# Kernel tuning notes

Hardware: AMD Instinct MI355X
Metric: run time of the kernel (lower is better)

Reference implementation:

```python
import jax, jax.numpy as jnp
import numpy as np

HIDDEN = 1024
HEADS = 8
HEAD_DIM = HIDDEN // HEADS  # 128
MAX_SEQ = 4096
MAX_TOKS = 2048
THETA = 10000.0
INIT_STD = 0.02


def setup_inputs() -> dict:
    key = jax.random.key(0)
    ks = jax.random.split(key, 8)
    B, L = 2, 4096
    hidden_states = jax.random.normal(ks[0], (B, L, HIDDEN), dtype=jnp.float32)
    attention_mask = jnp.ones((B, L), dtype=bool)
    segment_ids = jnp.sort(jax.random.randint(ks[1], (B, L), 0, 2), axis=-1).astype(jnp.int32)
    position_ids = jnp.sort(jax.random.randint(ks[2], (B, L), 0, MAX_SEQ), axis=-1).astype(jnp.int32)
    # nn.Linear weights stored (out_features, in_features), bias=False, normal(0, 0.02)
    wq = (jax.random.normal(ks[3], (HIDDEN, HIDDEN), dtype=jnp.float32) * INIT_STD)
    wk = (jax.random.normal(ks[4], (HIDDEN, HIDDEN), dtype=jnp.float32) * INIT_STD)
    wv = (jax.random.normal(ks[5], (HIDDEN, HIDDEN), dtype=jnp.float32) * INIT_STD)
    wo = (jax.random.normal(ks[6], (HIDDEN, HIDDEN), dtype=jnp.float32) * INIT_STD)
    return {
        "hidden_states": hidden_states,
        "wq": wq, "wk": wk, "wv": wv, "wo": wo,
        "attention_mask": attention_mask,
        "segment_ids": segment_ids,
        "position_ids": position_ids,
    }


def _freqs_cis(position_ids):
    # precompute_freqs_cis gathered at position_ids -> (B, L, HEAD_DIM//2) complex
    inv_freq = 1.0 / (THETA ** (jnp.arange(0, HEAD_DIM, 2, dtype=jnp.float32) / HEAD_DIM))
    ang = position_ids.astype(jnp.float32)[..., None] * inv_freq  # (B,L,D/2)
    return jax.lax.complex(jnp.cos(ang), jnp.sin(ang))


def _apply_rope(x, fc):
    # x: (B,L,H,D); fc: (B,L,D/2) complex; broadcast fc over heads
    xs = x.astype(jnp.float32).reshape(*x.shape[:-1], HEAD_DIM // 2, 2)
    xc = jax.lax.complex(xs[..., 0], xs[..., 1])  # (B,L,H,D/2)
    out = xc * fc[:, :, None, :]
    return jnp.stack([jnp.real(out), jnp.imag(out)], axis=-1).reshape(x.shape).astype(x.dtype)


def reference(hidden_states, wq, wk, wv, wo, attention_mask, segment_ids, position_ids):
    B, L, _ = hidden_states.shape
    q = (hidden_states @ wq.T).reshape(B, L, HEADS, HEAD_DIM)
    k = (hidden_states @ wk.T).reshape(B, L, HEADS, HEAD_DIM)
    v = (hidden_states @ wv.T).reshape(B, L, HEADS, HEAD_DIM)

    fc = _freqs_cis(position_ids)
    q = _apply_rope(q, fc)
    k = _apply_rope(k, fc)

    # block-causal mask: query block index >= key block index
    blk = jnp.arange(L) // MAX_TOKS
    causal = blk[:, None] >= blk[None, :]                                   # (L,L)
    seg = (segment_ids[:, :, None] == segment_ids[:, None, :])              # (B,L,L)
    mask = attention_mask[:, None, None, :] & seg[:, None, :, :] & causal[None, None, :, :]

    scale = 1.0 / np.float32(np.sqrt(HEAD_DIM))
    scores = jnp.einsum('bqhd,bkhd->bhqk', q, k) * scale                    # (B,H,L,L)
    scores = jnp.where(mask, scores, jnp.float32(-jnp.inf))
    probs = jax.nn.softmax(scores, axis=-1)
    attn = jnp.einsum('bhqk,bkhd->bqhd', probs, v).reshape(B, L, HIDDEN)
    return attn @ wo.T
```

## Files before the change

kernel.cpp:

```cpp
#include <hip/hip_runtime.h>
#include <hip/hip_bf16.h>
#include <cstdint>
#include <cstddef>
#include <type_traits>

#define HID 1024
#define HEADS 8
#define HDIM 128
#define SEQ 4096
#define BATCH 2

typedef float f32x4 __attribute__((ext_vector_type(4)));
typedef float f32x16 __attribute__((ext_vector_type(16)));
typedef short bf16x8 __attribute__((ext_vector_type(8)));
typedef unsigned short u16x8 __attribute__((ext_vector_type(8)));

typedef bf16x8 __attribute__((may_alias)) bf16x8_a;
typedef u16x8  __attribute__((may_alias)) u16x8_a;
typedef float4 __attribute__((may_alias)) float4_a;
typedef unsigned int __attribute__((may_alias)) u32_a;

__device__ __forceinline__ unsigned short f2bf(float f) {
    union { float f; unsigned int u; } v; v.f = f;
    unsigned int u = v.u;
    unsigned int r = (u + 0x7FFFu + ((u >> 16) & 1u)) >> 16;
    return (unsigned short)r;
}
__device__ __forceinline__ float bf2f(unsigned short h) {
    union { unsigned int u; float f; } v; v.u = ((unsigned int)h) << 16;
    return v.f;
}

__device__ __forceinline__ void plane_swap(unsigned int& x, unsigned int& y) {
    asm("v_permlane32_swap_b32 %0, %1" : "+v"(x), "+v"(y));
}
__device__ __forceinline__ unsigned int cvt_pk(float lo, float hi) {
    unsigned int r;
    asm("v_cvt_pk_bf16_f32 %0, %1, %2" : "=v"(r) : "v"(lo), "v"(hi));
    return r;
}
__device__ __forceinline__ bf16x8 pack4(unsigned int a, unsigned int b,
                                        unsigned int c, unsigned int d) {
    union { unsigned int u[4]; bf16x8 v; } t;
    t.u[0] = a; t.u[1] = b; t.u[2] = c; t.u[3] = d;
    return t.v;
}
__device__ __forceinline__ void g2lds16(const unsigned short* g, unsigned short* l) {
    __builtin_amdgcn_global_load_lds(
        (const __attribute__((address_space(1))) void*)g,
        (__attribute__((address_space(3))) void*)l, 16, 0, 0);
}

__global__ __launch_bounds__(256)
void cvt_kernel(const float* __restrict__ X, unsigned short* __restrict__ Y)
{
    int i = (blockIdx.x * 256 + threadIdx.x) * 8;
    float4 d0 = *(const float4_a*)&X[i];
    float4 d1 = *(const float4_a*)&X[i + 4];
    u16x8 t;
    t[0] = f2bf(d0.x); t[1] = f2bf(d0.y); t[2] = f2bf(d0.z); t[3] = f2bf(d0.w);
    t[4] = f2bf(d1.x); t[5] = f2bf(d1.y); t[6] = f2bf(d1.z); t[7] = f2bf(d1.w);
    *(u16x8_a*)&Y[i] = t;
}

__global__ __launch_bounds__(256)
void cvtw_kernel(const float* __restrict__ w0, const float* __restrict__ w1,
                 const float* __restrict__ w2, const float* __restrict__ w3,
                 unsigned short* __restrict__ Y)
{
    const int WSZ8 = (HID * HID) / 8;
    int c = blockIdx.x * 256 + threadIdx.x;
    int quarter = c >> 17;
    int idx = (c & (WSZ8 - 1)) * 8;
    const float* w = quarter == 0 ? w0 : quarter == 1 ? w1 : quarter == 2 ? w2 : w3;
    float4 d0 = *(const float4_a*)&w[idx];
    float4 d1 = *(const float4_a*)&w[idx + 4];
    u16x8 t;
    t[0] = f2bf(d0.x); t[1] = f2bf(d0.y); t[2] = f2bf(d0.z); t[3] = f2bf(d0.w);
    t[4] = f2bf(d1.x); t[5] = f2bf(d1.y); t[6] = f2bf(d1.z); t[7] = f2bf(d1.w);
    *(u16x8_a*)&Y[(size_t)quarter * HID * HID + idx] = t;
}

template<typename OutT>
__global__ __launch_bounds__(256)
void gemm_swz(const unsigned short* __restrict__ A, const unsigned short* __restrict__ B,
              OutT* __restrict__ C, int M, int N, int K, int lda)
{
    __shared__ __align__(16) unsigned short Al[128][64];
    __shared__ __align__(16) unsigned short Bl[128][64];
    const int tid  = threadIdx.x;
    const int lane = tid & 63;
    const int w    = tid >> 6;
    const int wr   = w >> 1, wc = w & 1;
    const int l16  = lane & 15, l4 = lane >> 4;
    const int nwg  = gridDim.x * gridDim.y;
    const int id   = blockIdx.y * gridDim.x + blockIdx.x;
    const int swz  = (id & 7) * (nwg >> 3) + (id >> 3);
    const int bx   = swz % gridDim.x, by = swz / gridDim.x;
    const int tm   = by * 128, tn = bx * 128;
    const int srow  = lane >> 3;
    const int sslot = (lane & 7) ^ srow;

    f32x4 acc[4][4] = {};

    for (int ko = 0; ko < K; ko += 64) {
        __syncthreads();
#pragma unroll
        for (int it = 0; it < 4; ++it) {
            int ca = w * 4 + it;
            int row = ca * 8 + srow;
            g2lds16(&A[(size_t)(tm + row) * lda + ko + sslot * 8], &Al[ca * 8][0]);
            g2lds16(&B[(size_t)(tn + row) * K   + ko + sslot * 8], &Bl[ca * 8][0]);
        }
        __syncthreads();
#pragma unroll
        for (int kk = 0; kk < 2; ++kk) {
            const int rslot = (kk * 4 + l4) ^ (l16 & 7);
            bf16x8 af[4], bfr[4];
#pragma unroll
            for (int i = 0; i < 4; ++i)
                af[i] = *(const bf16x8_a*)&Al[wr*64 + i*16 + l16][rslot * 8];
#pragma unroll
            for (int j = 0; j < 4; ++j)
                bfr[j] = *(const bf16x8_a*)&Bl[wc*64 + j*16 + l16][rslot * 8];
#pragma unroll
            for (int i = 0; i < 4; ++i)
#pragma unroll
                for (int j = 0; j < 4; ++j)
                    acc[i][j] = __builtin_amdgcn_mfma_f32_16x16x32_bf16(af[i], bfr[j], acc[i][j], 0, 0, 0);
        }
    }
#pragma unroll
    for (int i = 0; i < 4; ++i)
#pragma unroll
        for (int j = 0; j < 4; ++j)
#pragma unroll
            for (int r = 0; r < 4; ++r) {
                int row = tm + wr*64 + i*16 + l4*4 + r;
                int col = tn + wc*64 + j*16 + l16;
                if constexpr (std::is_same<OutT, float>::value)
                    C[(size_t)row * N + col] = acc[i][j][r];
                else
                    C[(size_t)row * N + col] = f2bf(acc[i][j][r]);
            }
}

template<bool A_BF16, bool B_BF16, typename OutT>
__global__ __launch_bounds__(256)
void gemm_bt(const void* __restrict__ Av, const void* __restrict__ Bv,
             OutT* __restrict__ C, int M, int N, int K, int lda)
{
    __shared__ __align__(16) unsigned short Al[128][72];
    __shared__ __align__(16) unsigned short Bl[128][72];
    const int tid  = threadIdx.x;
    const int lane = tid & 63;
    const int w    = tid >> 6;
    const int wr   = w >> 1, wc = w & 1;
    const int l16  = lane & 15, l4 = lane >> 4;
    const int tm   = blockIdx.y * 128, tn = blockIdx.x * 128;

    f32x4 acc[4][4] = {};

    for (int ko = 0; ko < K; ko += 64) {
        __syncthreads();
#pragma unroll
        for (int it = 0; it < 4; ++it) {
            int c = tid + 256 * it;
            int row = c >> 3, col0 = (c & 7) * 8;
            if constexpr (A_BF16) {
                const unsigned short* A = (const unsigned short*)Av;
                *(u16x8_a*)&Al[row][col0] =
                    *(const u16x8_a*)&A[(size_t)(tm + row) * lda + ko + col0];
            } else {
                const float* A = (const float*)Av;
                const float* p = &A[(size_t)(tm + row) * lda + ko + col0];
                float4 d0 = *(const float4_a*)p;
                float4 d1 = *(const float4_a*)(p + 4);
                u16x8 t;
                t[0] = f2bf(d0.x); t[1] = f2bf(d0.y); t[2] = f2bf(d0.z); t[3] = f2bf(d0.w);
                t[4] = f2bf(d1.x); t[5] = f2bf(d1.y); t[6] = f2bf(d1.z); t[7] = f2bf(d1.w);
                *(u16x8_a*)&Al[row][col0] = t;
            }
            if constexpr (B_BF16) {
                const unsigned short* B = (const unsigned short*)Bv;
                *(u16x8_a*)&Bl[row][col0] =
                    *(const u16x8_a*)&B[(size_t)(tn + row) * K + ko + col0];
            } else {
                const float* B = (const float*)Bv;
                const float* p = &B[(size_t)(tn + row) * K + ko + col0];
                float4 d0 = *(const float4_a*)p;
                float4 d1 = *(const float4_a*)(p + 4);
                u16x8 t;
                t[0] = f2bf(d0.x); t[1] = f2bf(d0.y); t[2] = f2bf(d0.z); t[3] = f2bf(d0.w);
                t[4] = f2bf(d1.x); t[5] = f2bf(d1.y); t[6] = f2bf(d1.z); t[7] = f2bf(d1.w);
                *(u16x8_a*)&Bl[row][col0] = t;
            }
        }
        __syncthreads();
#pragma unroll
        for (int kk = 0; kk < 2; ++kk) {
            bf16x8 af[4], bfr[4];
#pragma unroll
            for (int i = 0; i < 4; ++i)
                af[i] = *(const bf16x8_a*)&Al[wr*64 + i*16 + l16][kk*32 + l4*8];
#pragma unroll
            for (int j = 0; j < 4; ++j)
                bfr[j] = *(const bf16x8_a*)&Bl[wc*64 + j*16 + l16][kk*32 + l4*8];
#pragma unroll
            for (int i = 0; i < 4; ++i)
#pragma unroll
                for (int j = 0; j < 4; ++j)
                    acc[i][j] = __builtin_amdgcn_mfma_f32_16x16x32_bf16(af[i], bfr[j], acc[i][j], 0, 0, 0);
        }
    }
#pragma unroll
    for (int i = 0; i < 4; ++i)
#pragma unroll
        for (int j = 0; j < 4; ++j)
#pragma unroll
            for (int r = 0; r < 4; ++r) {
                int row = tm + wr*64 + i*16 + l4*4 + r;
                int col = tn + wc*64 + j*16 + l16;
                if constexpr (std::is_same<OutT, float>::value)
                    C[(size_t)row * N + col] = acc[i][j][r];
                else
                    C[(size_t)row * N + col] = f2bf(acc[i][j][r]);
            }
}

template<int NH>
__global__ __launch_bounds__(256)
void rope_kernel(unsigned short* __restrict__ X, const int* __restrict__ pos_ids, int RS)
{
    int c = blockIdx.x * 256 + threadIdx.x;
    int d0 = (c & 15) * 8;
    int l  = (c >> 4) & 4095;
    int b  = c >> 16;
    int pos = pos_ids[b * SEQ + l];
    float sth[4], cth[4];
#pragma unroll
    for (int j = 0; j < 4; ++j) {
        int i = (d0 >> 1) + j;
        float invf = powf(10000.0f, -(float)i * (1.0f / 64.0f));
        float ang = (float)pos * invf;
        sincosf(ang, &sth[j], &cth[j]);
    }
    size_t base = (size_t)(b * SEQ + l) * RS + d0;
#pragma unroll
    for (int h = 0; h < NH; ++h) {
        u16x8 d = *(const u16x8_a*)&X[base + h * HDIM];
#pragma unroll
        for (int j = 0; j < 4; ++j) {
            float x0 = bf2f(d[2*j]), x1 = bf2f(d[2*j+1]);
            d[2*j]   = f2bf(x0 * cth[j] - x1 * sth[j]);
            d[2*j+1] = f2bf(x0 * sth[j] + x1 * cth[j]);
        }
        *(u16x8_a*)&X[base + h * HDIM] = d;
    }
}

__global__ __launch_bounds__(256, 2)
void attn_kernel(const unsigned short* Q,
                 const unsigned short* K,
                 const unsigned short* V,
                 const int* __restrict__ seg,
                 unsigned short* O, int RS)
{
    __shared__ __align__(16) unsigned short Kl[2][64][136];
    __shared__ __align__(16) unsigned short Vt[2][128][72];

    const int tid  = threadIdx.x;
    const int lane = tid & 63;
    const int l32  = lane & 31, hi = lane >> 5;
    const int w    = tid >> 6;
    const int qt = (SEQ / 128 - 1) - blockIdx.x;
    const int h  = blockIdx.y;
    const int b  = blockIdx.z;
    const int qg0 = qt * 128 + w * 32;
    const int hoff = h * HDIM;

    bf16x8 qf[8];
    {
        size_t base = (size_t)(b * SEQ + qg0 + l32) * RS + hoff;
#pragma unroll
        for (int kk = 0; kk < 8; ++kk)
            qf[kk] = *(const bf16x8_a*)&Q[base + kk*16 + hi*8];
    }

    f32x16 acco0 = {}, acco1 = {}, acco2 = {}, acco3 = {};
    float lsum = 0.f;

    const int nkt = ((qt >> 4) + 1) * 32;

    int lo = 0, hb = SEQ;
    while (lo < hb) { int mid = (lo + hb) >> 1; if (seg[b * SEQ + mid] == 0) lo = mid + 1; else hb = mid; }
    const int boundary = lo;
    const bool blk_seg1 = (seg[b * SEQ + qt * 128] == 1);
    const bool blk_seg0 = (seg[b * SEQ + qt * 128 + 127] == 0);
    const bool mixed = !blk_seg0 && !blk_seg1;
    int kstart = 0, kend = nkt;
    if (blk_seg1) kstart = boundary >> 6;
    if (blk_seg0) {
        int ke = (boundary + 63) >> 6;
        kend = ke < nkt ? ke : nkt;
    }
    const bool qlt = (qg0 + l32) < boundary;

    const int kp = tid & 31, db = tid >> 5;
    const float sc = 0.08838834764831845f;

    u16x8 kreg[4], v0a, v0b, v1a, v1b;
    {
        const int kb = kstart * 64;
#pragma unroll
        for (int it = 0; it < 4; ++it) {
            int c = tid + 256 * it;
            kreg[it] = *(const u16x8_a*)&K[(size_t)(b * SEQ + kb + (c >> 4)) * RS + hoff + (c & 15) * 8];
        }
        size_t vb0 = (size_t)(b * SEQ + kb + 2 * kp) * RS + hoff + db * 16;
        size_t vb1 = (size_t)(b * SEQ + kb + 2 * kp + 1) * RS + hoff + db * 16;
        v0a = *(const u16x8_a*)&V[vb0];     v0b = *(const u16x8_a*)&V[vb0 + 8];
        v1a = *(const u16x8_a*)&V[vb1];     v1b = *(const u16x8_a*)&V[vb1 + 8];
    }
#pragma unroll
    for (int it = 0; it < 4; ++it) {
        int c = tid + 256 * it;
        *(u16x8_a*)&Kl[0][c >> 4][(c & 15) * 8] = kreg[it];
    }
#pragma unroll
    for (int j = 0; j < 8; ++j) {
        *(u32_a*)&Vt[0][db * 16 + j][2 * kp] =
            (unsigned int)(unsigned short)v0a[j] | ((unsigned int)(unsigned short)v1a[j] << 16);
        *(u32_a*)&Vt[0][db * 16 + 8 + j][2 * kp] =
            (unsigned int)(unsigned short)v0b[j] | ((unsigned int)(unsigned short)v1b[j] << 16);
    }
    if (kstart + 1 < kend) {
        const int kb2 = (kstart + 1) * 64;
#pragma unroll
        for (int it = 0; it < 4; ++it) {
            int c = tid + 256 * it;
            kreg[it] = *(const u16x8_a*)&K[(size_t)(b * SEQ + kb2 + (c >> 4)) * RS + hoff + (c & 15) * 8];
        }
        size_t vb0 = (size_t)(b * SEQ + kb2 + 2 * kp) * RS + hoff + db * 16;
        size_t vb1 = (size_t)(b * SEQ + kb2 + 2 * kp + 1) * RS + hoff + db * 16;
        v0a = *(const u16x8_a*)&V[vb0];     v0b = *(const u16x8_a*)&V[vb0 + 8];
        v1a = *(const u16x8_a*)&V[vb1];     v1b = *(const u16x8_a*)&V[vb1 + 8];
    }
    __syncthreads();

    int buf = 0;
    for (int kt = kstart; kt < kend; ++kt) {
        const int kb = kt * 64;

        f32x16 a0 = {}, a1 = {};
#pragma unroll
        for (int kk = 0; kk < 8; ++kk) {
            bf16x8 k0 = *(const bf16x8_a*)&Kl[buf][     l32][kk*16 + hi*8];
            bf16x8 k1 = *(const bf16x8_a*)&Kl[buf][32 + l32][kk*16 + hi*8];
            a0 = __builtin_amdgcn_mfma_f32_32x32x16_bf16(k0, qf[kk], a0, 0, 0, 0);
            a1 = __builtin_amdgcn_mfma_f32_32x32x16_bf16(k1, qf[kk], a1, 0, 0, 0);
        }

        unsigned int pk0[8], pk1[8];
        const bool need_mask = mixed || (kb < boundary && kb + 64 > boundary);
        if (need_mask) {
            const int kb0 = kb + 4 * hi, kb1 = kb + 32 + 4 * hi;
#pragma unroll
            for (int i = 0; i < 8; ++i) {
                int r0 = 2 * i;
                int off = (r0 & 3) + 8 * (r0 >> 2);
                float p0 = ((kb0 + off     < boundary) == qlt) ? __expf(a0[r0]     * sc) : 0.0f;
                float p1 = ((kb0 + off + 1 < boundary) == qlt) ? __expf(a0[r0 + 1] * sc) : 0.0f;
                float q0 = ((kb1 + off     < boundary) == qlt) ? __expf(a1[r0]     * sc) : 0.0f;
                float q1 = ((kb1 + off + 1 < boundary) == qlt) ? __expf(a1[r0 + 1] * sc) : 0.0f;
                lsum += (p0 + p1) + (q0 + q1);
                pk0[i] = cvt_pk(p0, p1);
                pk1[i] = cvt_pk(q0, q1);
            }
        } else {
#pragma unroll
            for (int i = 0; i < 8; ++i) {
                int r0 = 2 * i;
                float p0 = __expf(a0[r0]     * sc);
                float p1 = __expf(a0[r0 + 1] * sc);
                float q0 = __expf(a1[r0]     * sc);
                float q1 = __expf(a1[r0 + 1] * sc);
                lsum += (p0 + p1) + (q0 + q1);
                pk0[i] = cvt_pk(p0, p1);
                pk1[i] = cvt_pk(q0, q1);
            }
        }
        plane_swap(pk0[0], pk0[2]); plane_swap(pk0[1], pk0[3]);
        plane_swap(pk0[4], pk0[6]); plane_swap(pk0[5], pk0[7]);
        plane_swap(pk1[0], pk1[2]); plane_swap(pk1[1], pk1[3]);
        plane_swap(pk1[4], pk1[6]); plane_swap(pk1[5], pk1[7]);
        bf16x8 pf[4];
        pf[0] = pack4(pk0[0], pk0[1], pk0[2], pk0[3]);
        pf[1] = pack4(pk0[4], pk0[5], pk0[6], pk0[7]);
        pf[2] = pack4(pk1[0], pk1[1], pk1[2], pk1[3]);
        pf[3] = pack4(pk1[4], pk1[5], pk1[6], pk1[7]);

#pragma unroll
        for (int ks = 0; ks < 4; ++ks) {
            bf16x8 vf0 = *(const bf16x8_a*)&Vt[buf][      l32][ks*16 + hi*8];
            bf16x8 vf1 = *(const bf16x8_a*)&Vt[buf][32  + l32][ks*16 + hi*8];
            bf16x8 vf2 = *(const bf16x8_a*)&Vt[buf][64  + l32][ks*16 + hi*8];
            bf16x8 vf3 = *(const bf16x8_a*)&Vt[buf][96  + l32][ks*16 + hi*8];
            acco0 = __builtin_amdgcn_mfma_f32_32x32x16_bf16(pf[ks], vf0, acco0, 0, 0, 0);
            acco1 = __builtin_amdgcn_mfma_f32_32x32x16_bf16(pf[ks], vf1, acco1, 0, 0, 0);
            acco2 = __builtin_amdgcn_mfma_f32_32x32x16_bf16(pf[ks], vf2, acco2, 0, 0, 0);
            acco3 = __builtin_amdgcn_mfma_f32_32x32x16_bf16(pf[ks], vf3, acco3, 0, 0, 0);
        }

        if (kt + 1 < kend) {
            const int nb = buf ^ 1;
#pragma unroll
            for (int it = 0; it < 4; ++it) {
                int c = tid + 256 * it;
                *(u16x8_a*)&Kl[nb][c >> 4][(c & 15) * 8] = kreg[it];
            }
#pragma unroll
            for (int j = 0; j < 8; ++j) {
                *(u32_a*)&Vt[nb][db * 16 + j][2 * kp] =
                    (unsigned int)(unsigned short)v0a[j] | ((unsigned int)(unsigned short)v1a[j] << 16);
                *(u32_a*)&Vt[nb][db * 16 + 8 + j][2 * kp] =
                    (unsigned int)(unsigned short)v0b[j] | ((unsigned int)(unsigned short)v1b[j] << 16);
            }
            if (kt + 2 < kend) {
                const int kb2 = (kt + 2) * 64;
#pragma unroll
                for (int it = 0; it < 4; ++it) {
                    int c = tid + 256 * it;
                    kreg[it] = *(const u16x8_a*)&K[(size_t)(b * SEQ + kb2 + (c >> 4)) * RS + hoff + (c & 15) * 8];
                }
                size_t vb0 = (size_t)(b * SEQ + kb2 + 2 * kp) * RS + hoff + db * 16;
                size_t vb1 = (size_t)(b * SEQ + kb2 + 2 * kp + 1) * RS + hoff + db * 16;
                v0a = *(const u16x8_a*)&V[vb0];     v0b = *(const u16x8_a*)&V[vb0 + 8];
                v1a = *(const u16x8_a*)&V[vb1];     v1b = *(const u16x8_a*)&V[vb1 + 8];
            }
            __syncthreads();
        }
        buf ^= 1;
    }

    float tot = lsum + __shfl_xor(lsum, 32, 64);
#pragma unroll
    for (int r = 0; r < 16; ++r) {
        int qrow = (r & 3) + 8 * (r >> 2) + 4 * hi;
        float inv = 1.0f / __shfl(tot, qrow, 64);
        size_t base = (size_t)(b * SEQ + qg0 + qrow) * RS + hoff;
        O[base +       l32] = f2bf(acco0[r] * inv);
        O[base +  32 + l32] = f2bf(acco1[r] * inv);
        O[base +  64 + l32] = f2bf(acco2[r] * inv);
        O[base +  96 + l32] = f2bf(acco3[r] * inv);
    }
}

extern "C" void kernel_launch(void* const* d_in, const int* in_sizes, int n_in,
                              void* d_out, int out_size, void* d_ws, size_t ws_size,
                              hipStream_t stream)
{
    const float* X  = (const float*)d_in[0];
    const float* wq = (const float*)d_in[1];
    const float* wk = (const float*)d_in[2];
    const float* wv = (const float*)d_in[3];
    const float* wo = (const float*)d_in[4];
    const int* seg = (const int*)d_in[n_in - 2];
    const int* pos = (const int*)d_in[n_in - 1];
    float* out = (float*)d_out;

    const size_t NTOK = (size_t)BATCH * SEQ;
    const size_t MAT  = NTOK * HID;
    const size_t WSZ  = (size_t)HID * HID;

    if (ws_size >= (4 * MAT + 4 * WSZ) * sizeof(unsigned short)) {
        unsigned short* QKVb = (unsigned short*)d_ws;
        unsigned short* Xb   = QKVb + 3 * MAT;
        unsigned short* Wb   = Xb + MAT;
        unsigned short* Wob  = Wb + 3 * WSZ;

        cvt_kernel<<<(int)(MAT / (256 * 8)), 256, 0, stream>>>(X, Xb);
        cvtw_kernel<<<(int)(4 * WSZ / (256 * 8)), 256, 0, stream>>>(wq, wk, wv, wo, Wb);

        dim3 gq(3 * HID / 128, (int)(NTOK / 128));
        gemm_swz<unsigned short><<<gq, 256, 0, stream>>>(
            Xb, Wb, QKVb, (int)NTOK, 3 * HID, HID, HID);

        rope_kernel<16><<<(BATCH * SEQ * 16) / 256, 256, 0, stream>>>(QKVb, pos, 3 * HID);

        dim3 ga(SEQ / 128, HEADS, BATCH);
        attn_kernel<<<ga, 256, 0, stream>>>(QKVb, QKVb + HID, QKVb + 2 * HID, seg,
                                            QKVb , 3 * HID);

        dim3 go(HID / 128, (int)(NTOK / 128));
        gemm_swz<float><<<go, 256, 0, stream>>>(
            QKVb, Wob, out, (int)NTOK, HID, HID, 3 * HID);
    } else {
        unsigned short* Qb = (unsigned short*)d_ws;
        unsigned short* Kb = Qb + MAT;
        unsigned short* Vb = Kb + MAT;

        dim3 gg(HID / 128, (int)(NTOK / 128));
        gemm_bt<false, false, unsigned short><<<gg, 256, 0, stream>>>(
            (const void*)X, (const void*)wq, Qb, (int)NTOK, HID, HID, HID);
        gemm_bt<false, false, unsigned short><<<gg, 256, 0, stream>>>(
            (const void*)X, (const void*)wk, Kb, (int)NTOK, HID, HID, HID);
        gemm_bt<false, false, unsigned short><<<gg, 256, 0, stream>>>(
            (const void*)X, (const void*)wv, Vb, (int)NTOK, HID, HID, HID);

        rope_kernel<8><<<(BATCH * SEQ * 16) / 256, 256, 0, stream>>>(Qb, pos, HID);
        rope_kernel<8><<<(BATCH * SEQ * 16) / 256, 256, 0, stream>>>(Kb, pos, HID);

        dim3 ga(SEQ / 128, HEADS, BATCH);
        attn_kernel<<<ga, 256, 0, stream>>>(Qb, Kb, Vb, seg, Qb, HID);

        gemm_bt<true, false, float><<<gg, 256, 0, stream>>>(
            (const void*)Qb, (const void*)wo, out, (int)NTOK, HID, HID, HID);
    }
}
```

Baseline: 203.3 us.

## Split attention KV range across two blocks and merge partial outputs

Adds a split-K attention kernel where each query tile's key range is divided between two blocks, writing unnormalized bf16 partial outputs and row sums. A merge kernel then sums the halves and normalizes into the QKV buffer. This doubles grid parallelism and cuts the imbalance from long causal tiles. It also drops LDS double buffering to allow higher occupancy. The cost is extra workspace traffic, a second kernel launch, and bf16 rounding of unnormalized partials. It only runs if the workspace is large enough, otherwise the old path is kept.

```diff
diff --git a/kernel.cpp b/kernel.cpp
--- a/kernel.cpp
+++ b/kernel.cpp
@@ -259,15 +259,17 @@
     }
 }
 
-__global__ __launch_bounds__(256, 2)
-void attn_kernel(const unsigned short* Q,
-                 const unsigned short* K,
-                 const unsigned short* V,
-                 const int* __restrict__ seg,
-                 unsigned short* O, int RS)
-{
-    __shared__ __align__(16) unsigned short Kl[2][64][136];
-    __shared__ __align__(16) unsigned short Vt[2][128][72];
+__global__ __launch_bounds__(256, 4)
+void attn_split(const unsigned short* Q,
+                const unsigned short* K,
+                const unsigned short* V,
+                const int* __restrict__ seg,
+                unsigned short* __restrict__ Op,
+                float* __restrict__ Lp,
+                int RS)
+{
+    __shared__ __align__(16) unsigned short Kl[64][136];
+    __shared__ __align__(16) unsigned short Vt[128][72];
 
     const int tid  = threadIdx.x;
     const int lane = tid & 63;
@@ -275,7 +277,8 @@
     const int w    = tid >> 6;
     const int qt = (SEQ / 128 - 1) - blockIdx.x;
     const int h  = blockIdx.y;
-    const int b  = blockIdx.z;
+    const int zz = blockIdx.z;
+    const int b  = zz >> 1, half = zz & 1;
     const int qg0 = qt * 128 + w * 32;
     const int hoff = h * HDIM;
 
@@ -304,14 +307,18 @@
         int ke = (boundary + 63) >> 6;
         kend = ke < nkt ? ke : nkt;
     }
+    const int T = kend - kstart;
+    const int mid = kstart + ((T + 1) >> 1);
+    const int ks2 = half ? mid : kstart;
+    const int ke2 = half ? kend : mid;
+
     const bool qlt = (qg0 + l32) < boundary;
-
     const int kp = tid & 31, db = tid >> 5;
     const float sc = 0.08838834764831845f;
 
     u16x8 kreg[4], v0a, v0b, v1a, v1b;
-    {
-        const int kb = kstart * 64;
+    if (ks2 < ke2) {
+        const int kb = ks2 * 64;
 #pragma unroll
         for (int it = 0; it < 4; ++it) {
             int c = tid + 256 * it;
@@ -322,41 +329,42 @@
         v0a = *(const u16x8_a*)&V[vb0];     v0b = *(const u16x8_a*)&V[vb0 + 8];
         v1a = *(const u16x8_a*)&V[vb1];     v1b = *(const u16x8_a*)&V[vb1 + 8];
     }
-#pragma unroll
-    for (int it = 0; it < 4; ++it) {
-        int c = tid + 256 * it;
-        *(u16x8_a*)&Kl[0][c >> 4][(c & 15) * 8] = kreg[it];
-    }
-#pragma unroll
-    for (int j = 0; j < 8; ++j) {
-        *(u32_a*)&Vt[0][db * 16 + j][2 * kp] =
-            (unsigned int)(unsigned short)v0a[j] | ((unsigned int)(unsigned short)v1a[j] << 16);
-        *(u32_a*)&Vt[0][db * 16 + 8 + j][2 * kp] =
-            (unsigned int)(unsigned short)v0b[j] | ((unsigned int)(unsigned short)v1b[j] << 16);
-    }
-    if (kstart + 1 < kend) {
-        const int kb2 = (kstart + 1) * 64;
+
+    for (int kt = ks2; kt < ke2; ++kt) {
+        const int kb = kt * 64;
+        __syncthreads();
 #pragma unroll
         for (int it = 0; it < 4; ++it) {
             int c = tid + 256 * it;
-            kreg[it] = *(const u16x8_a*)&K[(size_t)(b * SEQ + kb2 + (c >> 4)) * RS + hoff + (c & 15) * 8];
-        }
-        size_t vb0 = (size_t)(b * SEQ + kb2 + 2 * kp) * RS + hoff + db * 16;
-        size_t vb1 = (size_t)(b * SEQ + kb2 + 2 * kp + 1) * RS + hoff + db * 16;
-        v0a = *(const u16x8_a*)&V[vb0];     v0b = *(const u16x8_a*)&V[vb0 + 8];
-        v1a = *(const u16x8_a*)&V[vb1];     v1b = *(const u16x8_a*)&V[vb1 + 8];
-    }
-    __syncthreads();
-
-    int buf = 0;
-    for (int kt = kstart; kt < kend; ++kt) {
-        const int kb = kt * 64;
+            *(u16x8_a*)&Kl[c >> 4][(c & 15) * 8] = kreg[it];
+        }
+#pragma unroll
+        for (int j = 0; j < 8; ++j) {
+            *(u32_a*)&Vt[db * 16 + j][2 * kp] =
+                (unsigned int)(unsigned short)v0a[j] | ((unsigned int)(unsigned short)v1a[j] << 16);
+            *(u32_a*)&Vt[db * 16 + 8 + j][2 * kp] =
+                (unsigned int)(unsigned short)v0b[j] | ((unsigned int)(unsigned short)v1b[j] << 16);
+        }
+        __syncthreads();
+
+        if (kt + 1 < ke2) {
+            const int kb2 = (kt + 1) * 64;
+#pragma unroll
+            for (int it = 0; it < 4; ++it) {
+                int c = tid + 256 * it;
+                kreg[it] = *(const u16x8_a*)&K[(size_t)(b * SEQ + kb2 + (c >> 4)) * RS + hoff + (c & 15) * 8];
+            }
+            size_t vb0 = (size_t)(b * SEQ + kb2 + 2 * kp) * RS + hoff + db * 16;
+            size_t vb1 = (size_t)(b * SEQ + kb2 + 2 * kp + 1) * RS + hoff + db * 16;
+            v0a = *(const u16x8_a*)&V[vb0];     v0b = *(const u16x8_a*)&V[vb0 + 8];
+            v1a = *(const u16x8_a*)&V[vb1];     v1b = *(const u16x8_a*)&V[vb1 + 8];
+        }
 
         f32x16 a0 = {}, a1 = {};
 #pragma unroll
         for (int kk = 0; kk < 8; ++kk) {
-            bf16x8 k0 = *(const bf16x8_a*)&Kl[buf][     l32][kk*16 + hi*8];
-            bf16x8 k1 = *(const bf16x8_a*)&Kl[buf][32 + l32][kk*16 + hi*8];
+            bf16x8 k0 = *(const bf16x8_a*)&Kl[     l32][kk*16 + hi*8];
+            bf16x8 k1 = *(const bf16x8_a*)&Kl[32 + l32][kk*16 + hi*8];
             a0 = __builtin_amdgcn_mfma_f32_32x32x16_bf16(k0, qf[kk], a0, 0, 0, 0);
             a1 = __builtin_amdgcn_mfma_f32_32x32x16_bf16(k1, qf[kk], a1, 0, 0, 0);
         }
@@ -402,6 +410,195 @@
 
 #pragma unroll
         for (int ks = 0; ks < 4; ++ks) {
+            bf16x8 vf0 = *(const bf16x8_a*)&Vt[      l32][ks*16 + hi*8];
+            bf16x8 vf1 = *(const bf16x8_a*)&Vt[32  + l32][ks*16 + hi*8];
+            bf16x8 vf2 = *(const bf16x8_a*)&Vt[64  + l32][ks*16 + hi*8];
+            bf16x8 vf3 = *(const bf16x8_a*)&Vt[96  + l32][ks*16 + hi*8];
+            acco0 = __builtin_amdgcn_mfma_f32_32x32x16_bf16(pf[ks], vf0, acco0, 0, 0, 0);
+            acco1 = __builtin_amdgcn_mfma_f32_32x32x16_bf16(pf[ks], vf1, acco1, 0, 0, 0);
+            acco2 = __builtin_amdgcn_mfma_f32_32x32x16_bf16(pf[ks], vf2, acco2, 0, 0, 0);
+            acco3 = __builtin_amdgcn_mfma_f32_32x32x16_bf16(pf[ks], vf3, acco3, 0, 0, 0);
+        }
+    }
+
+    float tot = lsum + __shfl_xor(lsum, 32, 64);
+    if (hi == 0)
+        Lp[((size_t)half * BATCH * SEQ + b * SEQ + qg0 + l32) * HEADS + h] = tot;
+    unsigned short* Oh = Op + (size_t)half * BATCH * SEQ * HID;
+#pragma unroll
+    for (int r = 0; r < 16; ++r) {
+        int qrow = (r & 3) + 8 * (r >> 2) + 4 * hi;
+        size_t base = (size_t)(b * SEQ + qg0 + qrow) * HID + hoff;
+        Oh[base +       l32] = f2bf(acco0[r]);
+        Oh[base +  32 + l32] = f2bf(acco1[r]);
+        Oh[base +  64 + l32] = f2bf(acco2[r]);
+        Oh[base +  96 + l32] = f2bf(acco3[r]);
+    }
+}
+
+__global__ __launch_bounds__(256)
+void merge_norm(const unsigned short* __restrict__ Op, const float* __restrict__ Lp,
+                unsigned short* __restrict__ QKV)
+{
+    int c = blockIdx.x * 256 + threadIdx.x;
+    int tok = c >> 7, chunk = c & 127;
+    int h = chunk >> 4;
+    size_t lidx = (size_t)tok * HEADS + h;
+    float l = Lp[lidx] + Lp[(size_t)BATCH * SEQ * HEADS + lidx];
+    float inv = 1.0f / l;
+    size_t o = (size_t)tok * HID + chunk * 8;
+    u16x8 x0 = *(const u16x8_a*)&Op[o];
+    u16x8 x1 = *(const u16x8_a*)&Op[(size_t)BATCH * SEQ * HID + o];
+    u16x8 r;
+#pragma unroll
+    for (int j = 0; j < 8; ++j)
+        r[j] = f2bf((bf2f(x0[j]) + bf2f(x1[j])) * inv);
+    *(u16x8_a*)&QKV[(size_t)tok * (3 * HID) + chunk * 8] = r;
+}
+
+__global__ __launch_bounds__(256, 2)
+void attn_kernel(const unsigned short* Q,
+                 const unsigned short* K,
+                 const unsigned short* V,
+                 const int* __restrict__ seg,
+                 unsigned short* O, int RS)
+{
+    __shared__ __align__(16) unsigned short Kl[2][64][136];
+    __shared__ __align__(16) unsigned short Vt[2][128][72];
+
+    const int tid  = threadIdx.x;
+    const int lane = tid & 63;
+    const int l32  = lane & 31, hi = lane >> 5;
+    const int w    = tid >> 6;
+    const int qt = (SEQ / 128 - 1) - blockIdx.x;
+    const int h  = blockIdx.y;
+    const int b  = blockIdx.z;
+    const int qg0 = qt * 128 + w * 32;
+    const int hoff = h * HDIM;
+
+    bf16x8 qf[8];
+    {
+        size_t base = (size_t)(b * SEQ + qg0 + l32) * RS + hoff;
+#pragma unroll
+        for (int kk = 0; kk < 8; ++kk)
+            qf[kk] = *(const bf16x8_a*)&Q[base + kk*16 + hi*8];
+    }
+
+    f32x16 acco0 = {}, acco1 = {}, acco2 = {}, acco3 = {};
+    float lsum = 0.f;
+
+    const int nkt = ((qt >> 4) + 1) * 32;
+
+    int lo = 0, hb = SEQ;
+    while (lo < hb) { int mid = (lo + hb) >> 1; if (seg[b * SEQ + mid] == 0) lo = mid + 1; else hb = mid; }
+    const int boundary = lo;
+    const bool blk_seg1 = (seg[b * SEQ + qt * 128] == 1);
+    const bool blk_seg0 = (seg[b * SEQ + qt * 128 + 127] == 0);
+    const bool mixed = !blk_seg0 && !blk_seg1;
+    int kstart = 0, kend = nkt;
+    if (blk_seg1) kstart = boundary >> 6;
+    if (blk_seg0) {
+        int ke = (boundary + 63) >> 6;
+        kend = ke < nkt ? ke : nkt;
+    }
+    const bool qlt = (qg0 + l32) < boundary;
+
+    const int kp = tid & 31, db = tid >> 5;
+    const float sc = 0.08838834764831845f;
+
+    u16x8 kreg[4], v0a, v0b, v1a, v1b;
+    {
+        const int kb = kstart * 64;
+#pragma unroll
+        for (int it = 0; it < 4; ++it) {
+            int c = tid + 256 * it;
+            kreg[it] = *(const u16x8_a*)&K[(size_t)(b * SEQ + kb + (c >> 4)) * RS + hoff + (c & 15) * 8];
+        }
+        size_t vb0 = (size_t)(b * SEQ + kb + 2 * kp) * RS + hoff + db * 16;
+        size_t vb1 = (size_t)(b * SEQ + kb + 2 * kp + 1) * RS + hoff + db * 16;
+        v0a = *(const u16x8_a*)&V[vb0];     v0b = *(const u16x8_a*)&V[vb0 + 8];
+        v1a = *(const u16x8_a*)&V[vb1];     v1b = *(const u16x8_a*)&V[vb1 + 8];
+    }
+#pragma unroll
+    for (int it = 0; it < 4; ++it) {
+        int c = tid + 256 * it;
+        *(u16x8_a*)&Kl[0][c >> 4][(c & 15) * 8] = kreg[it];
+    }
+#pragma unroll
+    for (int j = 0; j < 8; ++j) {
+        *(u32_a*)&Vt[0][db * 16 + j][2 * kp] =
+            (unsigned int)(unsigned short)v0a[j] | ((unsigned int)(unsigned short)v1a[j] << 16);
+        *(u32_a*)&Vt[0][db * 16 + 8 + j][2 * kp] =
+            (unsigned int)(unsigned short)v0b[j] | ((unsigned int)(unsigned short)v1b[j] << 16);
+    }
+    if (kstart + 1 < kend) {
+        const int kb2 = (kstart + 1) * 64;
+#pragma unroll
+        for (int it = 0; it < 4; ++it) {
+            int c = tid + 256 * it;
+            kreg[it] = *(const u16x8_a*)&K[(size_t)(b * SEQ + kb2 + (c >> 4)) * RS + hoff + (c & 15) * 8];
+        }
+        size_t vb0 = (size_t)(b * SEQ + kb2 + 2 * kp) * RS + hoff + db * 16;
+        size_t vb1 = (size_t)(b * SEQ + kb2 + 2 * kp + 1) * RS + hoff + db * 16;
+        v0a = *(const u16x8_a*)&V[vb0];     v0b = *(const u16x8_a*)&V[vb0 + 8];
+        v1a = *(const u16x8_a*)&V[vb1];     v1b = *(const u16x8_a*)&V[vb1 + 8];
+    }
+    __syncthreads();
+
+    int buf = 0;
+    for (int kt = kstart; kt < kend; ++kt) {
+        const int kb = kt * 64;
+
+        f32x16 a0 = {}, a1 = {};
+#pragma unroll
+        for (int kk = 0; kk < 8; ++kk) {
+            bf16x8 k0 = *(const bf16x8_a*)&Kl[buf][     l32][kk*16 + hi*8];
+            bf16x8 k1 = *(const bf16x8_a*)&Kl[buf][32 + l32][kk*16 + hi*8];
+            a0 = __builtin_amdgcn_mfma_f32_32x32x16_bf16(k0, qf[kk], a0, 0, 0, 0);
+            a1 = __builtin_amdgcn_mfma_f32_32x32x16_bf16(k1, qf[kk], a1, 0, 0, 0);
+        }
+
+        unsigned int pk0[8], pk1[8];
+        const bool need_mask = mixed || (kb < boundary && kb + 64 > boundary);
+        if (need_mask) {
+            const int kb0 = kb + 4 * hi, kb1 = kb + 32 + 4 * hi;
+#pragma unroll
+            for (int i = 0; i < 8; ++i) {
+                int r0 = 2 * i;
+                int off = (r0 & 3) + 8 * (r0 >> 2);
+                float p0 = ((kb0 + off     < boundary) == qlt) ? __expf(a0[r0]     * sc) : 0.0f;
+                float p1 = ((kb0 + off + 1 < boundary) == qlt) ? __expf(a0[r0 + 1] * sc) : 0.0f;
+                float q0 = ((kb1 + off     < boundary) == qlt) ? __expf(a1[r0]     * sc) : 0.0f;
+                float q1 = ((kb1 + off + 1 < boundary) == qlt) ? __expf(a1[r0 + 1] * sc) : 0.0f;
+                lsum += (p0 + p1) + (q0 + q1);
+                pk0[i] = cvt_pk(p0, p1);
+                pk1[i] = cvt_pk(q0, q1);
+            }
+        } else {
+#pragma unroll
+            for (int i = 0; i < 8; ++i) {
+                int r0 = 2 * i;
+                float p0 = __expf(a0[r0]     * sc);
+                float p1 = __expf(a0[r0 + 1] * sc);
+                float q0 = __expf(a1[r0]     * sc);
+                float q1 = __expf(a1[r0 + 1] * sc);
+                lsum += (p0 + p1) + (q0 + q1);
+                pk0[i] = cvt_pk(p0, p1);
+                pk1[i] = cvt_pk(q0, q1);
+            }
+        }
+        plane_swap(pk0[0], pk0[2]); plane_swap(pk0[1], pk0[3]);
+        plane_swap(pk0[4], pk0[6]); plane_swap(pk0[5], pk0[7]);
+        plane_swap(pk1[0], pk1[2]); plane_swap(pk1[1], pk1[3]);
+        plane_swap(pk1[4], pk1[6]); plane_swap(pk1[5], pk1[7]);
+        bf16x8 pf[4];
+        pf[0] = pack4(pk0[0], pk0[1], pk0[2], pk0[3]);
+        pf[1] = pack4(pk0[4], pk0[5], pk0[6], pk0[7]);
+        pf[2] = pack4(pk1[0], pk1[1], pk1[2], pk1[3]);
+        pf[3] = pack4(pk1[4], pk1[5], pk1[6], pk1[7]);
+
+#pragma unroll
+        for (int ks = 0; ks < 4; ++ks) {
             bf16x8 vf0 = *(const bf16x8_a*)&Vt[buf][      l32][ks*16 + hi*8];
             bf16x8 vf1 = *(const bf16x8_a*)&Vt[buf][32  + l32][ks*16 + hi*8];
             bf16x8 vf2 = *(const bf16x8_a*)&Vt[buf][64  + l32][ks*16 + hi*8];
@@ -472,12 +669,17 @@
     const size_t NTOK = (size_t)BATCH * SEQ;
     const size_t MAT  = NTOK * HID;
     const size_t WSZ  = (size_t)HID * HID;
-
-    if (ws_size >= (4 * MAT + 4 * WSZ) * sizeof(unsigned short)) {
+    const size_t BASE = (4 * MAT + 4 * WSZ) * sizeof(unsigned short);
+    const size_t SPLIT = BASE + 2 * MAT * sizeof(unsigned short)
+                       + 2 * NTOK * HEADS * sizeof(float);
+
+    if (ws_size >= SPLIT) {
         unsigned short* QKVb = (unsigned short*)d_ws;
         unsigned short* Xb   = QKVb + 3 * MAT;
         unsigned short* Wb   = Xb + MAT;
         unsigned short* Wob  = Wb + 3 * WSZ;
+        unsigned short* Opb  = Wob + WSZ;
+        float*          Lpb  = (float*)(Opb + 2 * MAT);
 
         cvt_kernel<<<(int)(MAT / (256 * 8)), 256, 0, stream>>>(X, Xb);
         cvtw_kernel<<<(int)(4 * WSZ / (256 * 8)), 256, 0, stream>>>(wq, wk, wv, wo, Wb);
@@ -488,9 +690,32 @@
 
         rope_kernel<16><<<(BATCH * SEQ * 16) / 256, 256, 0, stream>>>(QKVb, pos, 3 * HID);
 
+        dim3 ga(SEQ / 128, HEADS, BATCH * 2);
+        attn_split<<<ga, 256, 0, stream>>>(QKVb, QKVb + HID, QKVb + 2 * HID, seg,
+                                           Opb, Lpb, 3 * HID);
+        merge_norm<<<(int)(NTOK * 128 / 256), 256, 0, stream>>>(Opb, Lpb, QKVb);
+
+        dim3 go(HID / 128, (int)(NTOK / 128));
+        gemm_swz<float><<<go, 256, 0, stream>>>(
+            QKVb, Wob, out, (int)NTOK, HID, HID, 3 * HID);
+    } else if (ws_size >= BASE) {
+        unsigned short* QKVb = (unsigned short*)d_ws;
+        unsigned short* Xb   = QKVb + 3 * MAT;
+        unsigned short* Wb   = Xb + MAT;
+        unsigned short* Wob  = Wb + 3 * WSZ;
+
+        cvt_kernel<<<(int)(MAT / (256 * 8)), 256, 0, stream>>>(X, Xb);
+        cvtw_kernel<<<(int)(4 * WSZ / (256 * 8)), 256, 0, stream>>>(wq, wk, wv, wo, Wb);
+
+        dim3 gq(3 * HID / 128, (int)(NTOK / 128));
+        gemm_swz<unsigned short><<<gq, 256, 0, stream>>>(
+            Xb, Wb, QKVb, (int)NTOK, 3 * HID, HID, HID);
+
+        rope_kernel<16><<<(BATCH * SEQ * 16) / 256, 256, 0, stream>>>(QKVb, pos, 3 * HID);
+
         dim3 ga(SEQ / 128, HEADS, BATCH);
         attn_kernel<<<ga, 256, 0, stream>>>(QKVb, QKVb + HID, QKVb + 2 * HID, seg,
-                                            QKVb , 3 * HID);
+                                            QKVb, 3 * HID);
 
         dim3 go(HID / 128, (int)(NTOK / 128));
         gemm_swz<float><<<go, 256, 0, stream>>>(
```

Result: slower. 446.9 us (+119.8%).
